# Kernel optimization log

Measured on AMD Instinct MI355X. Metric: run time of the kernel, lower is better.

## Reference

```python
import jax, jax.numpy as jnp
import numpy as np

EMBED = 256
HEADS = 8
HEAD_DIM = 32
MLP_DIM = 1024
NEG = -1e9  # large negative in place of -inf so fully-deselected rows don't NaN
LN_EPS = 1e-5


def _layernorm(x, g, b):
    m = jnp.mean(x, axis=-1, keepdims=True)
    v = jnp.mean(jnp.square(x - m), axis=-1, keepdims=True)
    return (x - m) / jnp.sqrt(v + LN_EPS) * g + b


def setup_inputs() -> dict:
    key = jax.random.key(0)
    ks = jax.random.split(key, 16)
    b, s, d = 64, 360, EMBED
    sc = 0.02
    return {
        "x": jax.random.normal(ks[0], (b, s, d), dtype=jnp.float32),
        "attention_mask": jnp.zeros((b, 1, 1, s), dtype=jnp.float32),
        # TokenRouter.weight_predictor: Linear(256, 1)
        "wp_w": jax.random.normal(ks[1], (1, d), dtype=jnp.float32) * sc,
        "wp_b": jnp.zeros((1,), dtype=jnp.float32),
        # TokenRouter.aux_predictor: Linear(256,128) -> SiLU -> Linear(128,2)
        "a1_w": jax.random.normal(ks[2], (d // 2, d), dtype=jnp.float32) * sc,
        "a1_b": jnp.zeros((d // 2,), dtype=jnp.float32),
        "a2_w": jax.random.normal(ks[3], (2, d // 2), dtype=jnp.float32) * sc,
        "a2_b": jnp.zeros((2,), dtype=jnp.float32),
        # transformer block (pre-LN GPT2-style)
        "ln1_g": jnp.ones((d,), dtype=jnp.float32),
        "ln1_b": jnp.zeros((d,), dtype=jnp.float32),
        "wqkv": jax.random.normal(ks[4], (d, 3 * d), dtype=jnp.float32) * sc,
        "bqkv": jnp.zeros((3 * d,), dtype=jnp.float32),
        "wo": jax.random.normal(ks[5], (d, d), dtype=jnp.float32) * sc,
        "bo": jnp.zeros((d,), dtype=jnp.float32),
        "ln2_g": jnp.ones((d,), dtype=jnp.float32),
        "ln2_b": jnp.zeros((d,), dtype=jnp.float32),
        "w1": jax.random.normal(ks[6], (d, MLP_DIM), dtype=jnp.float32) * sc,
        "b1": jnp.zeros((MLP_DIM,), dtype=jnp.float32),
        "w2": jax.random.normal(ks[7], (MLP_DIM, d), dtype=jnp.float32) * sc,
        "b2": jnp.zeros((d,), dtype=jnp.float32),
    }


def reference(x, attention_mask, wp_w, wp_b, a1_w, a1_b, a2_w, a2_b,
              ln1_g, ln1_b, wqkv, bqkv, wo, bo, ln2_g, ln2_b, w1, b1, w2, b2):
    b, s, d = x.shape
    # --- router: per-token scalar weight ---
    weights = (x @ wp_w.T + wp_b).squeeze(-1)  # [b, s]
    # --- aux predictor selects tokens (eval path: argmax over 2 logits) ---
    h = jax.nn.silu(x @ a1_w.T + a1_b)
    aux_logits = h @ a2_w.T + a2_b            # [b, s, 2]
    sel = jnp.argmax(aux_logits, axis=-1).astype(bool)  # [b, s]
    # --- masked transformer block over the selected token subset.
    # Compacting tokens then attending == full-seq attention with deselected
    # keys masked out (LN/MLP/residual are position-wise), so vectorize:
    bias = attention_mask + jnp.where(sel, 0.0, NEG)[:, None, None, :]  # [b,1,1,s]
    hn = _layernorm(x, ln1_g, ln1_b)
    qkv = hn @ wqkv + bqkv
    q, k, v = jnp.split(qkv, 3, axis=-1)
    q = q.reshape(b, s, HEADS, HEAD_DIM)
    k = k.reshape(b, s, HEADS, HEAD_DIM)
    v = v.reshape(b, s, HEADS, HEAD_DIM)
    scores = jnp.einsum("bqhd,bkhd->bhqk", q, k) / np.sqrt(HEAD_DIM).astype(np.float32)
    scores = scores + bias                   # [b, h, s, s]
    attn = jax.nn.softmax(scores, axis=-1)
    ctx = jnp.einsum("bhqk,bkhd->bqhd", attn, v).reshape(b, s, d)
    h1 = x + (ctx @ wo + bo)
    h2n = _layernorm(h1, ln2_g, ln2_b)
    block_out = h1 + (jax.nn.gelu(h2n @ w1 + b1) @ w2 + b2)  # [b, s, d]
    # --- scatter-recombine: selected -> weighted block output, else passthrough
    out = jnp.where(sel[..., None], block_out * weights[..., None], x)
    avg_selected = jnp.sum(sel.astype(x.dtype)) / b
    return out, avg_selected
```

## Files before the change

### kernel.cpp

```cpp
#include <hip/hip_runtime.h>
#include <math.h>
#include <stdint.h>

#define TOKN 23040
#define BSZ 64
#define SEQ 360
#define DIM 256
#define NHD 8
#define HDD 32
#define MLPD 1024
#define NEGV -1e9f

typedef __attribute__((ext_vector_type(8))) short bf16x8;
typedef __attribute__((ext_vector_type(4))) float f32x4;

static __device__ __forceinline__ short f2bs(float f) {
  unsigned u = __builtin_bit_cast(unsigned, f);
  u += 0x7fffu + ((u >> 16) & 1u);
  return (short)(u >> 16);
}
static __device__ __forceinline__ float bf2f(short s) {
  unsigned u = ((unsigned)(unsigned short)s) << 16;
  return __builtin_bit_cast(float, u);
}
static __device__ __forceinline__ unsigned packbf(float a, float b) {
  return (unsigned)(unsigned short)f2bs(a) | ((unsigned)(unsigned short)f2bs(b) << 16);
}
static __device__ __forceinline__ void gl16(const short* g, short* l) {
  __builtin_amdgcn_global_load_lds(
      (const __attribute__((address_space(1))) unsigned int*)g,
      (__attribute__((address_space(3))) unsigned int*)l, 16, 0, 0);
}

__global__ __launch_bounds__(256) void mega_k(
    const float* __restrict__ x, const float* __restrict__ g,
    const float* __restrict__ b, const float* __restrict__ wpw,
    const float* __restrict__ wpb, short* __restrict__ outn,
    float* __restrict__ wout, float* __restrict__ outx,
    const float* __restrict__ a1w, const float* __restrict__ a1b,
    const float* __restrict__ a2w, const float* __restrict__ a2b,
    int* __restrict__ sel,
    const float* __restrict__ wqkv, const float* __restrict__ wo,
    const float* __restrict__ w1, const float* __restrict__ w2,
    short* __restrict__ wqkvt, short* __restrict__ wot,
    short* __restrict__ w1t, short* __restrict__ w2t) {
  __shared__ __align__(16) unsigned char smem[20992];
  int bid = blockIdx.x;
  int t = threadIdx.x;

  if (bid < 720) {
    float(*XT)[36] = (float(*)[36])smem;
    float(*WT)[128] = (float(*)[128])(smem + 4608);
    int m0 = bid * 32;
    int tx = t & 31, ty = t >> 5;
    float acc[4][4] = {};
    int r = t >> 3, c = (t & 7) * 4;
    int n2 = t >> 1, c2 = (t & 1) * 16;
    for (int k0 = 0; k0 < 256; k0 += 32) {
      float4 xa = *(const float4*)(x + (size_t)(m0 + r) * 256 + k0 + c);
      XT[c + 0][r] = xa.x; XT[c + 1][r] = xa.y; XT[c + 2][r] = xa.z; XT[c + 3][r] = xa.w;
#pragma unroll
      for (int j = 0; j < 4; j++) {
        float4 wv = *(const float4*)(a1w + (size_t)n2 * 256 + k0 + c2 + j * 4);
        WT[c2 + j * 4 + 0][n2] = wv.x;
        WT[c2 + j * 4 + 1][n2] = wv.y;
        WT[c2 + j * 4 + 2][n2] = wv.z;
        WT[c2 + j * 4 + 3][n2] = wv.w;
      }
      __syncthreads();
#pragma unroll 8
      for (int kk = 0; kk < 32; kk++) {
        float4 wv4 = *(const float4*)&WT[kk][tx * 4];
        float4 xv4 = *(const float4*)&XT[kk][ty * 4];
        float xr[4] = {xv4.x, xv4.y, xv4.z, xv4.w};
        float wr[4] = {wv4.x, wv4.y, wv4.z, wv4.w};
#pragma unroll
        for (int i = 0; i < 4; i++)
#pragma unroll
          for (int j = 0; j < 4; j++) acc[i][j] += xr[i] * wr[j];
      }
      __syncthreads();
    }
    float b1v[4], a20[4], a21[4];
#pragma unroll
    for (int j = 0; j < 4; j++) {
      int dim = tx * 4 + j;
      b1v[j] = a1b[dim];
      a20[j] = a2w[dim];
      a21[j] = a2w[128 + dim];
    }
    float bias0 = a2b[0], bias1 = a2b[1];
#pragma unroll
    for (int i = 0; i < 4; i++) {
      float l0 = 0.f, l1 = 0.f;
#pragma unroll
      for (int j = 0; j < 4; j++) {
        float v = acc[i][j] + b1v[j];
        float h = v / (1.f + expf(-v));
        l0 += h * a20[j];
        l1 += h * a21[j];
      }
#pragma unroll
      for (int o = 1; o < 32; o <<= 1) { l0 += __shfl_xor(l0, o); l1 += __shfl_xor(l1, o); }
      if (tx == 0) sel[m0 + ty * 4 + i] = (l1 + bias1 > l0 + bias0) ? 1 : 0;
    }
  } else if (bid < 1488) {
    float(*tile)[33] = (float(*)[33])smem;
    int b2 = bid - 720;
    const float* src;
    short* dst;
    int K, N, kt, nt;
    if (b2 < 192) {
      src = wqkv; dst = wqkvt; K = 256; N = 768; kt = b2 / 24; nt = b2 % 24;
    } else if (b2 < 256) {
      int bb = b2 - 192; src = wo; dst = wot; K = 256; N = 256; kt = bb >> 3; nt = bb & 7;
    } else if (b2 < 512) {
      int bb = b2 - 256; src = w1; dst = w1t; K = 256; N = 1024; kt = bb >> 5; nt = bb & 31;
    } else {
      int bb = b2 - 512; src = w2; dst = w2t; K = 1024; N = 256; kt = bb >> 3; nt = bb & 7;
    }
    int r = t >> 3, c4 = (t & 7) * 4;
    const float4 v = *(const float4*)(src + (size_t)(kt * 32 + r) * N + nt * 32 + c4);
    tile[c4 + 0][r] = v.x;
    tile[c4 + 1][r] = v.y;
    tile[c4 + 2][r] = v.z;
    tile[c4 + 3][r] = v.w;
    __syncthreads();
    union { short s[4]; uint2 u; } o;
    o.s[0] = f2bs(tile[r][c4 + 0]);
    o.s[1] = f2bs(tile[r][c4 + 1]);
    o.s[2] = f2bs(tile[r][c4 + 2]);
    o.s[3] = f2bs(tile[r][c4 + 3]);
    *(uint2*)(dst + (size_t)(nt * 32 + r) * K + kt * 32 + c4) = o.u;
  } else {
    int tok = (bid - 1488) * 4 + (t >> 6);
    int lane = t & 63;
    const float4 xv = *(const float4*)(x + (size_t)tok * DIM + lane * 4);
    *(float4*)(outx + (size_t)tok * DIM + lane * 4) = xv;
    float s = xv.x + xv.y + xv.z + xv.w;
    float s2 = xv.x * xv.x + xv.y * xv.y + xv.z * xv.z + xv.w * xv.w;
#pragma unroll
    for (int o = 1; o < 64; o <<= 1) { s += __shfl_xor(s, o); s2 += __shfl_xor(s2, o); }
    float m = s * (1.f / DIM);
    float var = fmaxf(s2 * (1.f / DIM) - m * m, 0.f);
    float rstd = rsqrtf(var + 1e-5f);
    float4 gv = *(const float4*)(g + lane * 4);
    float4 bv = *(const float4*)(b + lane * 4);
    uint2 pk;
    pk.x = packbf((xv.x - m) * rstd * gv.x + bv.x, (xv.y - m) * rstd * gv.y + bv.y);
    pk.y = packbf((xv.z - m) * rstd * gv.z + bv.z, (xv.w - m) * rstd * gv.w + bv.w);
    *(uint2*)(outn + (size_t)tok * DIM + lane * 4) = pk;
    float4 wv = *(const float4*)(wpw + lane * 4);
    float wd = xv.x * wv.x + xv.y * wv.y + xv.z * wv.z + xv.w * wv.w;
#pragma unroll
    for (int o = 1; o < 64; o <<= 1) wd += __shfl_xor(wd, o);
    if (lane == 0) wout[tok] = wd + wpb[0];
  }
}

__global__ __launch_bounds__(512) void scan_k(
    const int* __restrict__ sel, int* __restrict__ g_idx,
    int* __restrict__ startp, int* __restrict__ cntp,
    int* __restrict__ mtotp, float* __restrict__ outavg) {
  __shared__ int sc[512];
  __shared__ int red[8];
  int b = blockIdx.x, t = threadIdx.x;
  int lane = t & 63, wave = t >> 6;
  int part = 0;
  for (int i = t; i < b * SEQ; i += 512) part += sel[i];
#pragma unroll
  for (int o = 1; o < 64; o <<= 1) part += __shfl_xor(part, o);
  if (lane == 0) red[wave] = part;
  __syncthreads();
  int start = 0;
#pragma unroll
  for (int w = 0; w < 8; w++) start += red[w];
  __syncthreads();
  int flag = (t < SEQ) ? sel[b * SEQ + t] : 0;
  sc[t] = flag;
  __syncthreads();
  int val = flag;
  for (int off = 1; off < 512; off <<= 1) {
    int add = (t >= off) ? sc[t - off] : 0;
    __syncthreads();
    val += add;
    sc[t] = val;
    __syncthreads();
  }
  if (flag) g_idx[start + val - 1] = b * SEQ + t;
  if (t == 511) { startp[b] = start; cntp[b] = val; }
  if (b == 63) {
    int mt = start + sc[511];
    if (t == 0) { *mtotp = mt; outavg[0] = (float)mt / 64.0f; }
    int e = mt + 256;
    if (e > TOKN) e = TOKN;
    for (int i = mt + t; i < e; i += 512) g_idx[i] = 0;
  }
}

template <int MODE, int BN>
__global__ __launch_bounds__(256) void gemm128_k(
    const short* __restrict__ A, const short* __restrict__ Bt,
    const float* __restrict__ bias, const float* __restrict__ resf,
    const short* __restrict__ resb, const float* __restrict__ wgt,
    const int* __restrict__ g_idx, const int* __restrict__ mtotp,
    short* __restrict__ outb, float* __restrict__ outf, int Ndim, int Kdim) {
  int Mt = *mtotp;
  int m0 = blockIdx.y * 128;
  if (m0 >= Mt) return;
  __shared__ __align__(16) short As0[128 * 32];
  __shared__ __align__(16) short As1[128 * 32];
  __shared__ __align__(16) short Bs0[BN * 32];
  __shared__ __align__(16) short Bs1[BN * 32];
  constexpr int NJ = BN / 32;
  int n0 = blockIdx.x * BN;
  int t = threadIdx.x;
  int wave = t >> 6, lane = t & 63;
  int l15 = lane & 15, quad = lane >> 4;
  int wr = (wave >> 1) * 64, wc = (wave & 1) * (BN / 2);
  int r0 = t >> 2, c0 = (t & 3) * 8;
  long arA = (MODE == 0) ? g_idx[m0 + r0] : (m0 + r0);
  long arB = (MODE == 0) ? g_idx[m0 + 64 + r0] : (m0 + 64 + r0);
  const short* gA0 = A + arA * Kdim + c0;
  const short* gA1 = A + arB * Kdim + c0;
  const short* gB0 = Bt + (size_t)(n0 + r0) * Kdim + c0;
  const short* gB1 = Bt + (size_t)(n0 + 64 + r0) * Kdim + c0;
  short* lA0 = As0 + wave * 512;
  short* lA1 = As1 + wave * 512;
  short* lB0 = Bs0 + wave * 512;
  short* lB1 = Bs1 + wave * 512;

  f32x4 acc[4][NJ];
#pragma unroll
  for (int i = 0; i < 4; i++)
#pragma unroll
    for (int j = 0; j < NJ; j++)
#pragma unroll
      for (int r = 0; r < 4; r++) acc[i][j][r] = 0.f;

  for (int k0 = 0; k0 < Kdim; k0 += 64) {
    gl16(gA0 + k0, lA0);
    gl16(gA1 + k0, lA0 + 2048);
    gl16(gA0 + k0 + 32, lA1);
    gl16(gA1 + k0 + 32, lA1 + 2048);
    gl16(gB0 + k0, lB0);
    gl16(gB0 + k0 + 32, lB1);
    if constexpr (BN == 128) {
      gl16(gB1 + k0, lB0 + 2048);
      gl16(gB1 + k0 + 32, lB1 + 2048);
    }
    __syncthreads();
    bf16x8 af[4], bfr[NJ];
#pragma unroll
    for (int i = 0; i < 4; i++)
      af[i] = *(const bf16x8*)&As0[(wr + i * 16 + l15) * 32 + quad * 8];
#pragma unroll
    for (int j = 0; j < NJ; j++)
      bfr[j] = *(const bf16x8*)&Bs0[(wc + j * 16 + l15) * 32 + quad * 8];
#pragma unroll
    for (int i = 0; i < 4; i++)
#pragma unroll
      for (int j = 0; j < NJ; j++)
        acc[i][j] = __builtin_amdgcn_mfma_f32_16x16x32_bf16(af[i], bfr[j],
                                                            acc[i][j], 0, 0, 0);
#pragma unroll
    for (int i = 0; i < 4; i++)
      af[i] = *(const bf16x8*)&As1[(wr + i * 16 + l15) * 32 + quad * 8];
#pragma unroll
    for (int j = 0; j < NJ; j++)
      bfr[j] = *(const bf16x8*)&Bs1[(wc + j * 16 + l15) * 32 + quad * 8];
#pragma unroll
    for (int i = 0; i < 4; i++)
#pragma unroll
      for (int j = 0; j < NJ; j++)
        acc[i][j] = __builtin_amdgcn_mfma_f32_16x16x32_bf16(af[i], bfr[j],
                                                            acc[i][j], 0, 0, 0);
    __syncthreads();
  }

#pragma unroll
  for (int i = 0; i < 4; i++) {
#pragma unroll
    for (int j = 0; j < NJ; j++) {
      int col = n0 + wc + j * 16 + l15;
      float bcol = bias[col];
#pragma unroll
      for (int r = 0; r < 4; r++) {
        int row = m0 + wr + i * 16 + quad * 4 + r;
        float v = acc[i][j][r] + bcol;
        size_t idx = (size_t)row * Ndim + col;
        if (MODE == 0) {
          outb[idx] = f2bs(v);
        } else if (MODE == 2) {
          float u = 0.7978845608028654f * (v + 0.044715f * v * v * v);
          float e = __expf(2.f * u);
          float th = 1.f - 2.f / (e + 1.f);
          outb[idx] = f2bs(0.5f * v * (1.f + th));
        } else {
          if (row < Mt) {
            int orig = g_idx[row];
            float o = (v + bf2f(resb[idx])) * wgt[orig];
            outf[(size_t)orig * 256 + col] = o;
          }
        }
      }
    }
  }
}

__global__ __launch_bounds__(256) void wo_ln_k(
    const short* __restrict__ A, const short* __restrict__ Bt,
    const float* __restrict__ bias, const float* __restrict__ resf,
    const float* __restrict__ g2, const float* __restrict__ b2,
    const int* __restrict__ g_idx, const int* __restrict__ mtotp,
    short* __restrict__ h1b, short* __restrict__ h2n) {
  int Mt = *mtotp;
  int m0 = blockIdx.x * 128;
  if (m0 >= Mt) return;
  __shared__ __align__(16) short As0[128 * 32];
  __shared__ __align__(16) short As1[128 * 32];
  __shared__ __align__(16) short Bs0[256 * 32];
  __shared__ __align__(16) short Bs1[256 * 32];
  __shared__ float ps[128][2], ps2[128][2];
  int t = threadIdx.x;
  int wave = t >> 6, lane = t & 63;
  int l15 = lane & 15, quad = lane >> 4;
  int wr = (wave >> 1) * 64, wc = (wave & 1) * 128;
  int r0 = t >> 2, c0 = (t & 3) * 8;
  const short* gA0 = A + (size_t)(m0 + r0) * 256 + c0;
  const short* gA1 = A + (size_t)(m0 + 64 + r0) * 256 + c0;
  const short* gB0 = Bt + (size_t)r0 * 256 + c0;
  short* lA0 = As0 + wave * 512;
  short* lA1 = As1 + wave * 512;
  short* lB0 = Bs0 + wave * 512;
  short* lB1 = Bs1 + wave * 512;

  f32x4 acc[4][8];
#pragma unroll
  for (int i = 0; i < 4; i++)
#pragma unroll
    for (int j = 0; j < 8; j++)
#pragma unroll
      for (int r = 0; r < 4; r++) acc[i][j][r] = 0.f;

  for (int k0 = 0; k0 < 256; k0 += 64) {
    gl16(gA0 + k0, lA0);
    gl16(gA1 + k0, lA0 + 2048);
    gl16(gA0 + k0 + 32, lA1);
    gl16(gA1 + k0 + 32, lA1 + 2048);
#pragma unroll
    for (int q = 0; q < 4; q++) {
      gl16(gB0 + (size_t)q * 64 * 256 + k0, lB0 + q * 2048);
      gl16(gB0 + (size_t)q * 64 * 256 + k0 + 32, lB1 + q * 2048);
    }
    __syncthreads();
    bf16x8 af[4], bfr[8];
#pragma unroll
    for (int i = 0; i < 4; i++)
      af[i] = *(const bf16x8*)&As0[(wr + i * 16 + l15) * 32 + quad * 8];
#pragma unroll
    for (int j = 0; j < 8; j++)
      bfr[j] = *(const bf16x8*)&Bs0[(wc + j * 16 + l15) * 32 + quad * 8];
#pragma unroll
    for (int i = 0; i < 4; i++)
#pragma unroll
      for (int j = 0; j < 8; j++)
        acc[i][j] = __builtin_amdgcn_mfma_f32_16x16x32_bf16(af[i], bfr[j],
                                                            acc[i][j], 0, 0, 0);
#pragma unroll
    for (int i = 0; i < 4; i++)
      af[i] = *(const bf16x8*)&As1[(wr + i * 16 + l15) * 32 + quad * 8];
#pragma unroll
    for (int j = 0; j < 8; j++)
      bfr[j] = *(const bf16x8*)&Bs1[(wc + j * 16 + l15) * 32 + quad * 8];
#pragma unroll
    for (int i = 0; i < 4; i++)
#pragma unroll
      for (int j = 0; j < 8; j++)
        acc[i][j] = __builtin_amdgcn_mfma_f32_16x16x32_bf16(af[i], bfr[j],
                                                            acc[i][j], 0, 0, 0);
    __syncthreads();
  }

  float bcol[8], gcol[8], bbcol[8];
#pragma unroll
  for (int j = 0; j < 8; j++) {
    int col = wc + j * 16 + l15;
    bcol[j] = bias[col];
    gcol[j] = g2[col];
    bbcol[j] = b2[col];
  }
  float s1v[4][4], s2v[4][4];
#pragma unroll
  for (int i = 0; i < 4; i++) {
#pragma unroll
    for (int r = 0; r < 4; r++) {
      int row = m0 + wr + i * 16 + quad * 4 + r;
      int orig = g_idx[row];
      const float* xr = resf + (size_t)orig * 256;
      float ls_ = 0.f, ls2_ = 0.f;
#pragma unroll
      for (int j = 0; j < 8; j++) {
        int col = wc + j * 16 + l15;
        float h1 = acc[i][j][r] + bcol[j] + xr[col];
        acc[i][j][r] = h1;
        h1b[(size_t)row * 256 + col] = f2bs(h1);
        ls_ += h1;
        ls2_ += h1 * h1;
      }
      s1v[i][r] = ls_;
      s2v[i][r] = ls2_;
    }
  }
#pragma unroll
  for (int i = 0; i < 4; i++)
#pragma unroll
    for (int r = 0; r < 4; r++) {
#pragma unroll
      for (int o = 1; o < 16; o <<= 1) {
        s1v[i][r] += __shfl_xor(s1v[i][r], o);
        s2v[i][r] += __shfl_xor(s2v[i][r], o);
      }
    }
  if (l15 == 0) {
#pragma unroll
    for (int i = 0; i < 4; i++)
#pragma unroll
      for (int r = 0; r < 4; r++) {
        int lr = wr + i * 16 + quad * 4 + r;
        ps[lr][wave & 1] = s1v[i][r];
        ps2[lr][wave & 1] = s2v[i][r];
      }
  }
  __syncthreads();
#pragma unroll
  for (int i = 0; i < 4; i++) {
#pragma unroll
    for (int r = 0; r < 4; r++) {
      int lr = wr + i * 16 + quad * 4 + r;
      float S = ps[lr][0] + ps[lr][1];
      float S2 = ps2[lr][0] + ps2[lr][1];
      float m = S * (1.f / 256.f);
      float var = fmaxf(S2 * (1.f / 256.f) - m * m, 0.f);
      float rstd = rsqrtf(var + 1e-5f);
      int row = m0 + lr;
#pragma unroll
      for (int j = 0; j < 8; j++) {
        int col = wc + j * 16 + l15;
        float h2 = (acc[i][j][r] - m) * rstd * gcol[j] + bbcol[j];
        h2n[(size_t)row * 256 + col] = f2bs(h2);
      }
    }
  }
}

__global__ __launch_bounds__(256) void attn_k(
    const short* __restrict__ qkv, const float* __restrict__ amask,
    const int* __restrict__ g_idx, const int* __restrict__ startp,
    const int* __restrict__ cntp, short* __restrict__ ctx) {
  __shared__ __align__(16) short VF[2 * 12 * 64 * 8];
  __shared__ __align__(16) float ls[384];
  int bh = blockIdx.x >> 1, qhalf = blockIdx.x & 1;
  int bb = bh >> 3, h = bh & 7;
  int t = threadIdx.x;
  int start = startp[bb], cnt = cntp[bb];
  size_t base = (size_t)start * 768;
  for (int i = t; i < 1536; i += 256) {
    int k = i >> 2, cg = (i & 3) * 8;
    union { int4 v; short s[8]; } u;
    if (k < cnt) {
      u.v = *(const int4*)(qkv + base + (size_t)k * 768 + 512 + h * 32 + cg);
    } else {
      u.v = make_int4(0, 0, 0, 0);
    }
    int c = k >> 5, qd = (k >> 3) & 3, j = k & 7;
#pragma unroll
    for (int jj = 0; jj < 8; jj++) {
      int d = cg + jj;
      VF[((((d >> 4) * 12 + c) * 64) + qd * 16 + (d & 15)) * 8 + j] = u.s[jj];
    }
  }
  for (int i = t; i < 384; i += 256)
    ls[i] = (i < cnt) ? amask[g_idx[start + i]] : 0.f;
  __syncthreads();

  int wave = t >> 6, lane = t & 63;
  int ql = lane & 15, quad = lane >> 4;
  int addr0 = (((quad & 1) * 2) * 16 + ql) * 4;
  int addr1 = addr0 + 64;
  bool hiq = quad >= 2;
  int nt = (cnt + 15) >> 4;
  int nc = (cnt + 31) >> 5;

  for (int qt = qhalf + 2 * wave; qt < nt; qt += 8) {
    int q0 = qt * 16, qrow = q0 + ql;
    bf16x8 qf;
#pragma unroll
    for (int j = 0; j < 8; j++) qf[j] = 0;
    if (qrow < cnt)
      qf = *(const bf16x8*)(qkv + base + (size_t)qrow * 768 + h * 32 + quad * 8);

    f32x4 o0, o1;
#pragma unroll
    for (int r = 0; r < 4; r++) { o0[r] = 0.f; o1[r] = 0.f; }
    float lsum = 0.f;

    for (int c = 0; c < nc; c++) {
      int keyA = c * 32 + ql;
      int keyB = keyA + 16;
      bf16x8 kfA, kfB;
#pragma unroll
      for (int j = 0; j < 8; j++) { kfA[j] = 0; kfB[j] = 0; }
      if (keyA < cnt)
        kfA = *(const bf16x8*)(qkv + base + (size_t)keyA * 768 + 256 + h * 32 + quad * 8);
      if (keyB < cnt)
        kfB = *(const bf16x8*)(qkv + base + (size_t)keyB * 768 + 256 + h * 32 + quad * 8);
      f32x4 sa, sb;
#pragma unroll
      for (int r = 0; r < 4; r++) { sa[r] = 0.f; sb[r] = 0.f; }
      sa = __builtin_amdgcn_mfma_f32_16x16x32_bf16(kfA, qf, sa, 0, 0, 0);
      sb = __builtin_amdgcn_mfma_f32_16x16x32_bf16(kfB, qf, sb, 0, 0, 0);
      int kbase = c * 32 + quad * 4;
      float4 la = *(const float4*)&ls[kbase];
      float4 lb = *(const float4*)&ls[kbase + 16];
      float ea0 = (kbase + 0 < cnt) ? __expf(sa[0] * 0.17677669529663687f + la.x) : 0.f;
      float ea1 = (kbase + 1 < cnt) ? __expf(sa[1] * 0.17677669529663687f + la.y) : 0.f;
      float ea2 = (kbase + 2 < cnt) ? __expf(sa[2] * 0.17677669529663687f + la.z) : 0.f;
      float ea3 = (kbase + 3 < cnt) ? __expf(sa[3] * 0.17677669529663687f + la.w) : 0.f;
      float eb0 = (kbase + 16 < cnt) ? __expf(sb[0] * 0.17677669529663687f + lb.x) : 0.f;
      float eb1 = (kbase + 17 < cnt) ? __expf(sb[1] * 0.17677669529663687f + lb.y) : 0.f;
      float eb2 = (kbase + 18 < cnt) ? __expf(sb[2] * 0.17677669529663687f + lb.z) : 0.f;
      float eb3 = (kbase + 19 < cnt) ? __expf(sb[3] * 0.17677669529663687f + lb.w) : 0.f;
      lsum += (ea0 + ea1) + (ea2 + ea3) + (eb0 + eb1) + (eb2 + eb3);
      unsigned pA0 = packbf(ea0, ea1), pA1 = packbf(ea2, ea3);
      unsigned pB0 = packbf(eb0, eb1), pB1 = packbf(eb2, eb3);
      int s00 = __builtin_amdgcn_ds_bpermute(addr0, (int)pA0);
      int s10 = __builtin_amdgcn_ds_bpermute(addr0, (int)pB0);
      int s01 = __builtin_amdgcn_ds_bpermute(addr0, (int)pA1);
      int s11 = __builtin_amdgcn_ds_bpermute(addr0, (int)pB1);
      int s02 = __builtin_amdgcn_ds_bpermute(addr1, (int)pA0);
      int s12 = __builtin_amdgcn_ds_bpermute(addr1, (int)pB0);
      int s03 = __builtin_amdgcn_ds_bpermute(addr1, (int)pA1);
      int s13 = __builtin_amdgcn_ds_bpermute(addr1, (int)pB1);
      union { int i[4]; bf16x8 v; } pf;
      pf.i[0] = hiq ? s10 : s00;
      pf.i[1] = hiq ? s11 : s01;
      pf.i[2] = hiq ? s12 : s02;
      pf.i[3] = hiq ? s13 : s03;
      bf16x8 v0 = *(const bf16x8*)&VF[(c * 64 + lane) * 8];
      bf16x8 v1 = *(const bf16x8*)&VF[((12 + c) * 64 + lane) * 8];
      o0 = __builtin_amdgcn_mfma_f32_16x16x32_bf16(v0, pf.v, o0, 0, 0, 0);
      o1 = __builtin_amdgcn_mfma_f32_16x16x32_bf16(v1, pf.v, o1, 0, 0, 0);
    }
    lsum += __shfl_xor(lsum, 16);
    lsum += __shfl_xor(lsum, 32);
    float inv = 1.f / lsum;

    if (qrow < cnt) {
      size_t cb = ((size_t)(start + qrow)) * 256 + h * 32;
      uint2 w0, w1;
      w0.x = packbf(o0[0] * inv, o0[1] * inv);
      w0.y = packbf(o0[2] * inv, o0[3] * inv);
      w1.x = packbf(o1[0] * inv, o1[1] * inv);
      w1.y = packbf(o1[2] * inv, o1[3] * inv);
      *(uint2*)(ctx + cb + quad * 4) = w0;
      *(uint2*)(ctx + cb + 16 + quad * 4) = w1;
    }
  }
}

extern "C" void kernel_launch(void* const* d_in, const int* in_sizes, int n_in,
                              void* d_out, int out_size, void* d_ws,
                              size_t ws_size, hipStream_t stream) {
  const float* x = (const float*)d_in[0];
  const float* amask = (const float*)d_in[1];
  const float* wp_w = (const float*)d_in[2];
  const float* wp_b = (const float*)d_in[3];
  const float* a1_w = (const float*)d_in[4];
  const float* a1_b = (const float*)d_in[5];
  const float* a2_w = (const float*)d_in[6];
  const float* a2_b = (const float*)d_in[7];
  const float* ln1_g = (const float*)d_in[8];
  const float* ln1_b = (const float*)d_in[9];
  const float* wqkv = (const float*)d_in[10];
  const float* bqkv = (const float*)d_in[11];
  const float* wo = (const float*)d_in[12];
  const float* bo = (const float*)d_in[13];
  const float* ln2_g = (const float*)d_in[14];
  const float* ln2_b = (const float*)d_in[15];
  const float* w1 = (const float*)d_in[16];
  const float* b1 = (const float*)d_in[17];
  const float* w2 = (const float*)d_in[18];
  const float* b2 = (const float*)d_in[19];
  float* out = (float*)d_out;

  uint8_t* p = (uint8_t*)d_ws;
  float* weightsv = (float*)p; p += (size_t)TOKN * 4;
  int* selv = (int*)p;         p += (size_t)TOKN * 4;
  int* idxlv = (int*)p;        p += (size_t)TOKN * 4;
  int* gidxv = (int*)p;        p += (size_t)TOKN * 4;
  int* cntv = (int*)p;         p += 64 * 4;
  int* startv = (int*)p;       p += 64 * 4;
  int* mtotv = (int*)p;        p += 64 * 4;
  short* wqkvt = (short*)p;    p += (size_t)768 * 256 * 2;
  short* wot = (short*)p;      p += (size_t)256 * 256 * 2;
  short* w1t = (short*)p;      p += (size_t)1024 * 256 * 2;
  short* w2t = (short*)p;      p += (size_t)256 * 1024 * 2;
  short* h1bv = (short*)p;     p += (size_t)TOKN * 256 * 2;
  short* h2nv = (short*)p;     p += (size_t)TOKN * 256 * 2;
  short* ctxv = (short*)p;     p += (size_t)TOKN * 256 * 2;
  uint8_t* R = p;
  short* xnv = (short*)R;
  short* qkvv = (short*)(R + (size_t)TOKN * 256 * 2);
  short* actv = (short*)R;
  (void)idxlv;

  mega_k<<<dim3(7248), dim3(256), 0, stream>>>(
      x, ln1_g, ln1_b, wp_w, wp_b, xnv, weightsv, out,
      a1_w, a1_b, a2_w, a2_b, selv,
      wqkv, wo, w1, w2, wqkvt, wot, w1t, w2t);
  scan_k<<<dim3(64), dim3(512), 0, stream>>>(selv, gidxv, startv, cntv, mtotv,
                                             out + (size_t)TOKN * 256);
  gemm128_k<0, 128><<<dim3(6, 180), dim3(256), 0, stream>>>(
      xnv, wqkvt, bqkv, nullptr, nullptr, nullptr, gidxv, mtotv, qkvv, nullptr,
      768, 256);
  attn_k<<<dim3(1024), dim3(256), 0, stream>>>(qkvv, amask, gidxv, startv, cntv, ctxv);
  wo_ln_k<<<dim3(180), dim3(256), 0, stream>>>(ctxv, wot, bo, x, ln2_g, ln2_b,
                                               gidxv, mtotv, h1bv, h2nv);
  gemm128_k<2, 128><<<dim3(8, 180), dim3(256), 0, stream>>>(
      h2nv, w1t, b1, nullptr, nullptr, nullptr, gidxv, mtotv, actv, nullptr,
      1024, 256);
  gemm128_k<3, 64><<<dim3(4, 180), dim3(256), 0, stream>>>(
      actv, w2t, b2, nullptr, h1bv, weightsv, gidxv, mtotv, nullptr, out, 256, 1024);
}
```

Measured before the change: 253.5 us.

## Restructure router MLP as per-token wave-split dot products with 1024-thread blocks

The aux predictor section of the fused prologue kernel changes from an LDS-tiled 32-token outer-product GEMM to a scheme where each lane owns one token and each of 16 waves computes 8 hidden units. Weights are read as wave-uniform values, and the two logits are reduced across waves through shared memory. All sections now run in 1024-thread blocks that process four transpose tiles or 16 tokens each, which cuts the launch to 1992 blocks. The goal is to remove the LDS staging and barriers of the old tiled GEMM and the per-block overhead. The cost is that each lane streams a full strided row of x, and the larger blocks may limit occupancy or register budget.

```diff
diff --git a/kernel.cpp b/kernel.cpp
--- a/kernel.cpp
+++ b/kernel.cpp
@@ -32,7 +32,7 @@
       (__attribute__((address_space(3))) unsigned int*)l, 16, 0, 0);
 }
 
-__global__ __launch_bounds__(256) void mega_k(
+__global__ __launch_bounds__(1024) void mega_k(
     const float* __restrict__ x, const float* __restrict__ g,
     const float* __restrict__ b, const float* __restrict__ wpw,
     const float* __restrict__ wpb, short* __restrict__ outn,
@@ -44,82 +44,71 @@
     const float* __restrict__ w1, const float* __restrict__ w2,
     short* __restrict__ wqkvt, short* __restrict__ wot,
     short* __restrict__ w1t, short* __restrict__ w2t) {
-  __shared__ __align__(16) unsigned char smem[20992];
+  __shared__ __align__(16) unsigned char smem[16896];
   int bid = blockIdx.x;
   int t = threadIdx.x;
 
-  if (bid < 720) {
-    float(*XT)[36] = (float(*)[36])smem;
-    float(*WT)[128] = (float(*)[128])(smem + 4608);
-    int m0 = bid * 32;
-    int tx = t & 31, ty = t >> 5;
-    float acc[4][4] = {};
-    int r = t >> 3, c = (t & 7) * 4;
-    int n2 = t >> 1, c2 = (t & 1) * 16;
-    for (int k0 = 0; k0 < 256; k0 += 32) {
-      float4 xa = *(const float4*)(x + (size_t)(m0 + r) * 256 + k0 + c);
-      XT[c + 0][r] = xa.x; XT[c + 1][r] = xa.y; XT[c + 2][r] = xa.z; XT[c + 3][r] = xa.w;
-#pragma unroll
-      for (int j = 0; j < 4; j++) {
-        float4 wv = *(const float4*)(a1w + (size_t)n2 * 256 + k0 + c2 + j * 4);
-        WT[c2 + j * 4 + 0][n2] = wv.x;
-        WT[c2 + j * 4 + 1][n2] = wv.y;
-        WT[c2 + j * 4 + 2][n2] = wv.z;
-        WT[c2 + j * 4 + 3][n2] = wv.w;
+  if (bid < 360) {
+    int wv = t >> 6, lane = t & 63;
+    int wvu = __builtin_amdgcn_readfirstlane(wv);
+    int tok = bid * 64 + lane;
+    const float* __restrict__ xr = x + (size_t)tok * 256;
+    const float* __restrict__ W8 = a1w + (size_t)wvu * 8 * 256;
+    float acc[8];
+#pragma unroll
+    for (int j = 0; j < 8; j++) acc[j] = 0.f;
+#pragma unroll 2
+    for (int k0 = 0; k0 < 256; k0 += 8) {
+      float4 xa = *(const float4*)(xr + k0);
+      float4 xb = *(const float4*)(xr + k0 + 4);
+      float xv[8] = {xa.x, xa.y, xa.z, xa.w, xb.x, xb.y, xb.z, xb.w};
+#pragma unroll
+      for (int j = 0; j < 8; j++) {
+        const float* wrow = W8 + j * 256 + k0;
+#pragma unroll
+        for (int m = 0; m < 8; m++) acc[j] += wrow[m] * xv[m];
       }
-      __syncthreads();
-#pragma unroll 8
-      for (int kk = 0; kk < 32; kk++) {
-        float4 wv4 = *(const float4*)&WT[kk][tx * 4];
-        float4 xv4 = *(const float4*)&XT[kk][ty * 4];
-        float xr[4] = {xv4.x, xv4.y, xv4.z, xv4.w};
-        float wr[4] = {wv4.x, wv4.y, wv4.z, wv4.w};
-#pragma unroll
-        for (int i = 0; i < 4; i++)
-#pragma unroll
-          for (int j = 0; j < 4; j++) acc[i][j] += xr[i] * wr[j];
+    }
+    float l0 = 0.f, l1 = 0.f;
+#pragma unroll
+    for (int j = 0; j < 8; j++) {
+      int dim = wvu * 8 + j;
+      float v = acc[j] + a1b[dim];
+      float h = v / (1.f + expf(-v));
+      l0 += h * a2w[dim];
+      l1 += h * a2w[128 + dim];
+    }
+    float* red0 = (float*)smem;
+    float* red1 = (float*)(smem + 4096);
+    red0[wv * 64 + lane] = l0;
+    red1[wv * 64 + lane] = l1;
+    __syncthreads();
+    if (wv == 0) {
+      float s0 = 0.f, s1 = 0.f;
+#pragma unroll
+      for (int w = 0; w < 16; w++) {
+        s0 += red0[w * 64 + lane];
+        s1 += red1[w * 64 + lane];
       }
-      __syncthreads();
-    }
-    float b1v[4], a20[4], a21[4];
-#pragma unroll
-    for (int j = 0; j < 4; j++) {
-      int dim = tx * 4 + j;
-      b1v[j] = a1b[dim];
-      a20[j] = a2w[dim];
-      a21[j] = a2w[128 + dim];
-    }
-    float bias0 = a2b[0], bias1 = a2b[1];
-#pragma unroll
-    for (int i = 0; i < 4; i++) {
-      float l0 = 0.f, l1 = 0.f;
-#pragma unroll
-      for (int j = 0; j < 4; j++) {
-        float v = acc[i][j] + b1v[j];
-        float h = v / (1.f + expf(-v));
-        l0 += h * a20[j];
-        l1 += h * a21[j];
-      }
-#pragma unroll
-      for (int o = 1; o < 32; o <<= 1) { l0 += __shfl_xor(l0, o); l1 += __shfl_xor(l1, o); }
-      if (tx == 0) sel[m0 + ty * 4 + i] = (l1 + bias1 > l0 + bias0) ? 1 : 0;
-    }
-  } else if (bid < 1488) {
-    float(*tile)[33] = (float(*)[33])smem;
-    int b2 = bid - 720;
+      sel[tok] = (s1 + a2b[1] > s0 + a2b[0]) ? 1 : 0;
+    }
+  } else if (bid < 552) {
+    int sub = t >> 8, t256 = t & 255;
+    float(*tile)[33] = ((float(*)[33])smem) + sub * 32;
+    int tid = (bid - 360) * 4 + sub;
     const float* src;
     short* dst;
     int K, N, kt, nt;
-    if (b2 < 192) {
-      src = wqkv; dst = wqkvt; K = 256; N = 768; kt = b2 / 24; nt = b2 % 24;
-    } else if (b2 < 256) {
-      int bb = b2 - 192; src = wo; dst = wot; K = 256; N = 256; kt = bb >> 3; nt = bb & 7;
-    } else if (b2 < 512) {
-      int bb = b2 - 256; src = w1; dst = w1t; K = 256; N = 1024; kt = bb >> 5; nt = bb & 31;
+    if (tid < 192) {
+      src = wqkv; dst = wqkvt; K = 256; N = 768; kt = tid / 24; nt = tid % 24;
+    } else if (tid < 256) {
+      int bb = tid - 192; src = wo; dst = wot; K = 256; N = 256; kt = bb >> 3; nt = bb & 7;
+    } else if (tid < 512) {
+      int bb = tid - 256; src = w1; dst = w1t; K = 256; N = 1024; kt = bb >> 5; nt = bb & 31;
     } else {
-      int bb = b2 - 512; src = w2; dst = w2t; K = 1024; N = 256; kt = bb >> 3; nt = bb & 7;
-    }
-    int r = t >> 3, c4 = (t & 7) * 4;
+      int bb = tid - 512; src = w2; dst = w2t; K = 1024; N = 256; kt = bb >> 3; nt = bb & 7;
+    }
+    int r = t256 >> 3, c4 = (t256 & 7) * 4;
     const float4 v = *(const float4*)(src + (size_t)(kt * 32 + r) * N + nt * 32 + c4);
     tile[c4 + 0][r] = v.x;
     tile[c4 + 1][r] = v.y;
@@ -133,7 +122,7 @@
     o.s[3] = f2bs(tile[r][c4 + 3]);
     *(uint2*)(dst + (size_t)(nt * 32 + r) * K + kt * 32 + c4) = o.u;
   } else {
-    int tok = (bid - 1488) * 4 + (t >> 6);
+    int tok = (bid - 552) * 16 + (t >> 6);
     int lane = t & 63;
     const float4 xv = *(const float4*)(x + (size_t)tok * DIM + lane * 4);
     *(float4*)(outx + (size_t)tok * DIM + lane * 4) = xv;
@@ -615,7 +604,7 @@
   short* actv = (short*)R;
   (void)idxlv;
 
-  mega_k<<<dim3(7248), dim3(256), 0, stream>>>(
+  mega_k<<<dim3(1992), dim3(1024), 0, stream>>>(
       x, ln1_g, ln1_b, wp_w, wp_b, xnv, weightsv, out,
       a1_w, a1_b, a2_w, a2_b, selv,
       wqkv, wo, w1, w2, wqkvt, wot, w1t, w2t);
```

Result: slower. 282.2 us (+11.3%).

## Double-buffer LDS tiles in GEMM to prefetch next K-slice during MFMA

Applied to the files above, without the earlier changes.

The GEMM main loop used to load a 64-wide K chunk into two LDS buffers, synchronize, then compute on both halves. It now steps through K in 32-wide slices. Each iteration issues the global-to-LDS loads for the next slice into the alternate buffer before running the MFMAs on the current one, so load latency can overlap with compute. The cost is one barrier per 32-wide slice instead of per 64-wide chunk, and less load batching per step.

```diff
diff --git a/kernel.cpp b/kernel.cpp
--- a/kernel.cpp
+++ b/kernel.cpp
@@ -208,10 +208,8 @@
   int Mt = *mtotp;
   int m0 = blockIdx.y * 128;
   if (m0 >= Mt) return;
-  __shared__ __align__(16) short As0[128 * 32];
-  __shared__ __align__(16) short As1[128 * 32];
-  __shared__ __align__(16) short Bs0[BN * 32];
-  __shared__ __align__(16) short Bs1[BN * 32];
+  __shared__ __align__(16) short As[2][128 * 32];
+  __shared__ __align__(16) short Bs[2][BN * 32];
   constexpr int NJ = BN / 32;
   int n0 = blockIdx.x * BN;
   int t = threadIdx.x;
@@ -225,10 +223,7 @@
   const short* gA1 = A + arB * Kdim + c0;
   const short* gB0 = Bt + (size_t)(n0 + r0) * Kdim + c0;
   const short* gB1 = Bt + (size_t)(n0 + 64 + r0) * Kdim + c0;
-  short* lA0 = As0 + wave * 512;
-  short* lA1 = As1 + wave * 512;
-  short* lB0 = Bs0 + wave * 512;
-  short* lB1 = Bs1 + wave * 512;
+  int wbase = wave * 512;
 
   f32x4 acc[4][NJ];
 #pragma unroll
@@ -238,37 +233,33 @@
 #pragma unroll
       for (int r = 0; r < 4; r++) acc[i][j][r] = 0.f;
 
-  for (int k0 = 0; k0 < Kdim; k0 += 64) {
-    gl16(gA0 + k0, lA0);
-    gl16(gA1 + k0, lA0 + 2048);
-    gl16(gA0 + k0 + 32, lA1);
-    gl16(gA1 + k0 + 32, lA1 + 2048);
-    gl16(gB0 + k0, lB0);
-    gl16(gB0 + k0 + 32, lB1);
-    if constexpr (BN == 128) {
-      gl16(gB1 + k0, lB0 + 2048);
-      gl16(gB1 + k0 + 32, lB1 + 2048);
-    }
-    __syncthreads();
+  int nst = Kdim >> 5;
+  gl16(gA0, As[0] + wbase);
+  gl16(gA1, As[0] + 2048 + wbase);
+  gl16(gB0, Bs[0] + wbase);
+  if constexpr (BN == 128) gl16(gB1, Bs[0] + 2048 + wbase);
+  __syncthreads();
+
+  int buf = 0;
+  for (int s = 0; s < nst; ++s) {
+    if (s + 1 < nst) {
+      int off = (s + 1) * 32;
+      short* d = (buf ^ 1) ? &As[1][0] : &As[0][0];
+      short* e = (buf ^ 1) ? &Bs[1][0] : &Bs[0][0];
+      gl16(gA0 + off, d + wbase);
+      gl16(gA1 + off, d + 2048 + wbase);
+      gl16(gB0 + off, e + wbase);
+      if constexpr (BN == 128) gl16(gB1 + off, e + 2048 + wbase);
+    }
+    const short* Ab = buf ? &As[1][0] : &As[0][0];
+    const short* Bb = buf ? &Bs[1][0] : &Bs[0][0];
     bf16x8 af[4], bfr[NJ];
 #pragma unroll
     for (int i = 0; i < 4; i++)
-      af[i] = *(const bf16x8*)&As0[(wr + i * 16 + l15) * 32 + quad * 8];
+      af[i] = *(const bf16x8*)&Ab[(wr + i * 16 + l15) * 32 + quad * 8];
 #pragma unroll
     for (int j = 0; j < NJ; j++)
-      bfr[j] = *(const bf16x8*)&Bs0[(wc + j * 16 + l15) * 32 + quad * 8];
-#pragma unroll
-    for (int i = 0; i < 4; i++)
-#pragma unroll
-      for (int j = 0; j < NJ; j++)
-        acc[i][j] = __builtin_amdgcn_mfma_f32_16x16x32_bf16(af[i], bfr[j],
-                                                            acc[i][j], 0, 0, 0);
-#pragma unroll
-    for (int i = 0; i < 4; i++)
-      af[i] = *(const bf16x8*)&As1[(wr + i * 16 + l15) * 32 + quad * 8];
-#pragma unroll
-    for (int j = 0; j < NJ; j++)
-      bfr[j] = *(const bf16x8*)&Bs1[(wc + j * 16 + l15) * 32 + quad * 8];
+      bfr[j] = *(const bf16x8*)&Bb[(wc + j * 16 + l15) * 32 + quad * 8];
 #pragma unroll
     for (int i = 0; i < 4; i++)
 #pragma unroll
@@ -276,6 +267,7 @@
         acc[i][j] = __builtin_amdgcn_mfma_f32_16x16x32_bf16(af[i], bfr[j],
                                                             acc[i][j], 0, 0, 0);
     __syncthreads();
+    buf ^= 1;
   }
 
 #pragma unroll
```

Result: faster. 243.5 us (-4.0%).
